# Optimization experiments

Measured on AMD Instinct MI355X. Metric: run time of the kernel, lower is better.

Reference implementation:

```python
import jax, jax.numpy as jnp
import numpy as np

N = 50000
E = 1600000
IN_F = 512
OUT_F = 128
NEG_SLOPE = 0.01   # nn.LeakyReLU() default
TEMPERATURE = 0.5


def setup_inputs() -> dict:
    key = jax.random.key(0)
    k1, k2, k3, k4 = jax.random.split(key, 4)
    h = jax.random.normal(k1, (N, IN_F), dtype=jnp.float32)
    # xavier_uniform with gain=1.414
    limW = 1.414 * np.sqrt(6.0 / (IN_F + OUT_F))
    W = jax.random.uniform(k2, (IN_F, OUT_F), minval=-limW, maxval=limW, dtype=jnp.float32)
    lima = 1.414 * np.sqrt(6.0 / (2 * OUT_F + 1))
    a = jax.random.uniform(k3, (2 * OUT_F, 1), minval=-lima, maxval=lima, dtype=jnp.float32)
    edge_index = jax.random.randint(k4, (2, E), 0, N, dtype=jnp.int64)
    return {"h": h, "W": W, "a": a, "edge_index": edge_index}


def reference(h, W, a, edge_index):
    # Inference: F.dropout(training=False) is identity.
    Wh = h @ W                                   # [N, F_out]
    src = edge_index[0]                          # row indices -> softmax segments
    dst = edge_index[1]
    # cat([Wh[src], Wh[dst]]) @ a == (Wh @ a1)[src] + (Wh @ a2)[dst]
    a1 = a[:OUT_F, 0]
    a2 = a[OUT_F:, 0]
    s1 = Wh @ a1                                 # [N]
    s2 = Wh @ a2                                 # [N]
    e = s1[src] + s2[dst]                        # [E]
    e = jnp.where(e >= 0, e, NEG_SLOPE * e)      # LeakyReLU
    logits = e / TEMPERATURE
    # sparse softmax over dim=1 (per source-node row segments)
    seg_max = jax.ops.segment_max(logits, src, num_segments=N)  # [N]
    ex = jnp.exp(logits - seg_max[src])          # [E]
    denom = jax.ops.segment_sum(ex, src, num_segments=N)        # [N]
    att = ex / denom[src]                        # [E]
    # sparse-dense matmul: h_prime[i] = sum_j att(i,j) * Wh[j]
    h_prime = jax.ops.segment_sum(att[:, None] * Wh[dst], src, num_segments=N)  # [N, F_out]
    return jax.nn.relu(h_prime)                  # concat=True path
```

## Files before the change

kernel.cpp:

```cpp
#include <hip/hip_runtime.h>
#include <cstdint>
#include <cstddef>

#define N_NODES 50000
#define N_EDGES 1600000
#define IN_FEAT 512
#define OUT_FEAT 128
#define NEG_SLOPE 0.01f
#define INV_TEMP 2.0f
#define PAD_DEG 128

#define BUCKETS 400
#define BNODES 125
#define BCAP 5000
#define A_BLOCKS 250
#define A_EPC (N_EDGES / A_BLOCKS)
#define A_G4 (A_EPC / 4)

#define CONV_BLOCKS ((IN_FEAT * OUT_FEAT) / 256)
#define GEMM_BLOCKS ((N_NODES + 63) / 64)

typedef __attribute__((ext_vector_type(8))) short short8;
typedef __attribute__((ext_vector_type(4))) float f32x4;

#define GLOBAL_AS __attribute__((address_space(1)))
#define LDS_AS __attribute__((address_space(3)))

__device__ inline unsigned short f2bf(float x) {
    unsigned int u = __float_as_uint(x);
    unsigned int r = (u + 0x7fffu + ((u >> 16) & 1u)) >> 16;
    return (unsigned short)r;
}
__device__ inline float bf2f(unsigned short b) {
    return __uint_as_float(((unsigned int)b) << 16);
}


__global__ __launch_bounds__(256) void build_kernel(const float* __restrict__ W,
                                                    unsigned short* __restrict__ Wt,
                                                    const int* __restrict__ src,
                                                    const int* __restrict__ dst,
                                                    int* __restrict__ bucket_cursor,
                                                    int* __restrict__ binned) {
    __shared__ int cntL[BUCKETS];
    __shared__ int baseL[BUCKETS];

    if (blockIdx.x >= A_BLOCKS) {
        int tid = (blockIdx.x - A_BLOCKS) * 256 + threadIdx.x;
        if (tid < IN_FEAT * OUT_FEAT) {
            int n = tid >> 9;
            int k = tid & 511;
            Wt[tid] = f2bf(W[k * OUT_FEAT + n]);
        }
        return;
    }

    int t = threadIdx.x;
    for (int i = t; i < BUCKETS; i += 256) cntL[i] = 0;
    __syncthreads();
    size_t ebase = (size_t)blockIdx.x * A_EPC;

    for (int g = t; g < A_G4; g += 256) {
        int4 s4 = *(const int4*)(src + ebase + (size_t)g * 4);
#pragma unroll
        for (int j = 0; j < 4; ++j) {
            int s = (&s4.x)[j];
            atomicAdd(&cntL[s / BNODES], 1);
        }
    }
    __syncthreads();
    for (int i = t; i < BUCKETS; i += 256) {
        int c = cntL[i];
        baseL[i] = c ? atomicAdd(&bucket_cursor[i], c) : 0;
        cntL[i] = 0;
    }
    __syncthreads();
    for (int g = t; g < A_G4; g += 256) {
        int4 s4 = *(const int4*)(src + ebase + (size_t)g * 4);
        int4 d4 = *(const int4*)(dst + ebase + (size_t)g * 4);
#pragma unroll
        for (int j = 0; j < 4; ++j) {
            int s = (&s4.x)[j];
            int b = s / BNODES;
            int sl = s - b * BNODES;
            int pos = atomicAdd(&cntL[b], 1);
            int slot = baseL[b] + pos;
            if (slot < BCAP)
                binned[(size_t)b * BCAP + slot] = (sl << 16) | (&d4.x)[j];
        }
    }
}


__global__ __launch_bounds__(256) void gemm_binB_kernel(const float* __restrict__ h,
                                                        const unsigned short* __restrict__ Wt,
                                                        const float* __restrict__ a_vec,
                                                        unsigned short* __restrict__ Whb,
                                                        float* __restrict__ s1,
                                                        float* __restrict__ s2,
                                                        const int* __restrict__ bucket_cursor,
                                                        const int* __restrict__ binned,
                                                        int* __restrict__ cnt,
                                                        int* __restrict__ csr) {
    __shared__ unsigned short lB[2][8 * 2 * 64 * 8];

    if (blockIdx.x < BUCKETS) {
        int* cL = (int*)&lB[0][0];
        int b = blockIdx.x;
        int t = threadIdx.x;
        if (t < BNODES) cL[t] = 0;
        __syncthreads();
        int m = min(bucket_cursor[b], BCAP);
        const int* bp = binned + (size_t)b * BCAP;
        int n0 = b * BNODES;
        for (int i = t; i < m; i += 256) {
            int p = bp[i];
            int sl = p >> 16;
            int d = p & 0xFFFF;
            int pos = atomicAdd(&cL[sl], 1);
            if (pos < PAD_DEG) csr[(size_t)(n0 + sl) * PAD_DEG + pos] = d;
        }
        __syncthreads();
        if (t < BNODES) cnt[n0 + t] = min(cL[t], PAD_DEG);
        return;
    }

    int bid = blockIdx.x - BUCKETS;
    int t = threadIdx.x;
    int w = t >> 6;
    int L = t & 63;
    int m0 = bid * 64;

    int arow = m0 + w * 16 + (L & 15);
    bool arow_ok = arow < N_NODES;
    int kq = (L >> 4) * 8;
    const float* arp = h + (size_t)arow * IN_FEAT + kq;

    f32x4 acc[8];
#pragma unroll
    for (int i = 0; i < 8; ++i) acc[i] = (f32x4){0.f, 0.f, 0.f, 0.f};

    auto stageB = [&](int buf, int k0) {
#pragma unroll
        for (int c = 0; c < 4; ++c) {
            int nb = w * 2 + (c >> 1);
            int ksub = c & 1;
            const GLOBAL_AS unsigned short* g =
                (const GLOBAL_AS unsigned short*)(Wt + (size_t)(nb * 16 + (L & 15)) * IN_FEAT +
                                                  (k0 + ksub * 32 + kq));
            LDS_AS unsigned short* lp = (LDS_AS unsigned short*)(&lB[buf][(nb * 2 + ksub) * 512]);
            __builtin_amdgcn_global_load_lds((const GLOBAL_AS void*)g, (LDS_AS void*)lp, 16, 0, 0);
        }
    };

    float4 av[2][2];
#pragma unroll
    for (int c = 0; c < 2; ++c) {
        av[c][0] = make_float4(0.f, 0.f, 0.f, 0.f);
        av[c][1] = make_float4(0.f, 0.f, 0.f, 0.f);
    }
    if (arow_ok) {
        av[0][0] = *(const float4*)(arp);
        av[0][1] = *(const float4*)(arp + 4);
        av[1][0] = *(const float4*)(arp + 32);
        av[1][1] = *(const float4*)(arp + 36);
    }
    stageB(0, 0);
    __syncthreads();

#pragma unroll
    for (int it = 0; it < 8; ++it) {
        const int buf = it & 1;

        if (it < 7) stageB(buf ^ 1, (it + 1) * 64);

        float4 avn[2][2];
#pragma unroll
        for (int c = 0; c < 2; ++c) {
            avn[c][0] = make_float4(0.f, 0.f, 0.f, 0.f);
            avn[c][1] = make_float4(0.f, 0.f, 0.f, 0.f);
        }
        if (it < 7 && arow_ok) {
            const float* p = arp + (it + 1) * 64;
            avn[0][0] = *(const float4*)(p);
            avn[0][1] = *(const float4*)(p + 4);
            avn[1][0] = *(const float4*)(p + 32);
            avn[1][1] = *(const float4*)(p + 36);
        }

        short8 af[2];
#pragma unroll
        for (int c = 0; c < 2; ++c) {
            short8 v;
            v[0] = (short)f2bf(av[c][0].x); v[1] = (short)f2bf(av[c][0].y);
            v[2] = (short)f2bf(av[c][0].z); v[3] = (short)f2bf(av[c][0].w);
            v[4] = (short)f2bf(av[c][1].x); v[5] = (short)f2bf(av[c][1].y);
            v[6] = (short)f2bf(av[c][1].z); v[7] = (short)f2bf(av[c][1].w);
            af[c] = v;
        }

#pragma unroll
        for (int ksub = 0; ksub < 2; ++ksub) {
#pragma unroll
            for (int nb = 0; nb < 8; ++nb) {
                short8 bf = *(const short8*)(&lB[buf][((nb * 2 + ksub) * 64 + L) * 8]);
                acc[nb] = __builtin_amdgcn_mfma_f32_16x16x32_bf16(af[ksub], bf, acc[nb], 0, 0, 0);
            }
        }

        __syncthreads();
#pragma unroll
        for (int c = 0; c < 2; ++c) {
            av[c][0] = avn[c][0];
            av[c][1] = avn[c][1];
        }
    }

    int col0 = L & 15;
    int rbase = m0 + w * 16 + (L >> 4) * 4;

    float a1c[8], a2c[8];
#pragma unroll
    for (int nb = 0; nb < 8; ++nb) {
        a1c[nb] = a_vec[nb * 16 + col0];
        a2c[nb] = a_vec[128 + nb * 16 + col0];
    }

#pragma unroll
    for (int r = 0; r < 4; ++r) {
        int row = rbase + r;
        bool ok = row < N_NODES;
        float p1 = 0.f, p2 = 0.f;
        if (ok) {
            unsigned short* orow = Whb + (size_t)row * OUT_FEAT;
#pragma unroll
            for (int nb = 0; nb < 8; ++nb) {
                float v = acc[nb][r];
                orow[nb * 16 + col0] = f2bf(v);
                p1 = fmaf(v, a1c[nb], p1);
                p2 = fmaf(v, a2c[nb], p2);
            }
        }
#pragma unroll
        for (int off = 8; off > 0; off >>= 1) {
            p1 += __shfl_xor(p1, off, 64);
            p2 += __shfl_xor(p2, off, 64);
        }
        if (ok && col0 == 0) {
            s1[row] = p1;
            s2[row] = p2;
        }
    }
}


__global__ __launch_bounds__(256) void node_kernel(const unsigned short* __restrict__ Whb,
                                                   const float* __restrict__ s1,
                                                   const float* __restrict__ s2,
                                                   const int* __restrict__ cnt,
                                                   const int* __restrict__ csr,
                                                   float* __restrict__ out) {
    int lane = threadIdx.x & 63;
    int w = threadIdx.x >> 6;
    int n = blockIdx.x * 4 + w;
    if (n >= N_NODES) return;
    int deg = cnt[n];
    size_t start = (size_t)n * PAD_DEG;
    int g = lane >> 4;
    int fo = lane & 15;

    float accv[8];
#pragma unroll
    for (int f = 0; f < 8; ++f) accv[f] = 0.f;
    float inv = 0.f;

    if (deg > 0) {
        float s1n = s1[n];
        int d0 = 0, d1 = 0;
        float ex0 = 0.f, ex1 = 0.f;
        if (lane < deg) {
            d0 = csr[start + lane];
            float ev = s1n + s2[d0];
            ev = ev >= 0.f ? ev : NEG_SLOPE * ev;
            ex0 = __expf(ev * INV_TEMP);
        }
        if (lane + 64 < deg) {
            d1 = csr[start + lane + 64];
            float ev = s1n + s2[d1];
            ev = ev >= 0.f ? ev : NEG_SLOPE * ev;
            ex1 = __expf(ev * INV_TEMP);
        }
        float denom = ex0 + ex1;
#pragma unroll
        for (int off = 32; off > 0; off >>= 1) denom += __shfl_xor(denom, off, 64);
        inv = 1.0f / denom;

#pragma unroll 2
        for (int jj = 0; jj < deg; jj += 4) {
            int e = jj + g;
            bool hi = jj >= 64;
            float exs = hi ? ex1 : ex0;
            int dsel = hi ? d1 : d0;
            float p = __shfl(exs, e & 63, 64);
            int dd = __shfl(dsel, e & 63, 64);
            short8 row = *(const short8*)(Whb + (size_t)dd * OUT_FEAT + fo * 8);
#pragma unroll
            for (int f = 0; f < 8; ++f)
                accv[f] = fmaf(p, bf2f((unsigned short)row[f]), accv[f]);
        }
#pragma unroll
        for (int f = 0; f < 8; ++f) {
            accv[f] += __shfl_xor(accv[f], 16, 64);
            accv[f] += __shfl_xor(accv[f], 32, 64);
        }
    }

    if (g == 0) {
        float* orow = out + (size_t)n * OUT_FEAT + fo * 8;
        float4 o0, o1;
        o0.x = fmaxf(accv[0] * inv, 0.f); o0.y = fmaxf(accv[1] * inv, 0.f);
        o0.z = fmaxf(accv[2] * inv, 0.f); o0.w = fmaxf(accv[3] * inv, 0.f);
        o1.x = fmaxf(accv[4] * inv, 0.f); o1.y = fmaxf(accv[5] * inv, 0.f);
        o1.z = fmaxf(accv[6] * inv, 0.f); o1.w = fmaxf(accv[7] * inv, 0.f);
        *(float4*)(orow) = o0;
        *(float4*)(orow + 4) = o1;
    }
}


extern "C" void kernel_launch(void* const* d_in, const int* in_sizes, int n_in,
                              void* d_out, int out_size, void* d_ws, size_t ws_size,
                              hipStream_t stream) {
    const float* h = (const float*)d_in[0];
    const float* W = (const float*)d_in[1];
    const float* a = (const float*)d_in[2];
    const int* edge = (const int*)d_in[3];
    const int* src = edge;
    const int* dst = edge + N_EDGES;
    float* out = (float*)d_out;

    char* ws = (char*)d_ws;
    size_t off = 0;
    auto alloc = [&](size_t bytes) -> void* {
        void* p = ws + off;
        off = (off + bytes + 255) & ~(size_t)255;
        return p;
    };
    unsigned short* Whb = (unsigned short*)alloc((size_t)N_NODES * OUT_FEAT * sizeof(unsigned short));
    float* s1 = (float*)alloc((size_t)N_NODES * sizeof(float));
    float* s2 = (float*)alloc((size_t)N_NODES * sizeof(float));
    int* cnt = (int*)alloc((size_t)N_NODES * sizeof(int));
    int* csr = (int*)alloc((size_t)N_NODES * PAD_DEG * sizeof(int));
    unsigned short* Wt = (unsigned short*)alloc((size_t)IN_FEAT * OUT_FEAT * sizeof(unsigned short));
    int* bucket_cursor = (int*)alloc((size_t)BUCKETS * sizeof(int));
    int* binned = (int*)alloc((size_t)BUCKETS * BCAP * sizeof(int));

    hipMemsetAsync(bucket_cursor, 0, BUCKETS * sizeof(int), stream);
    build_kernel<<<A_BLOCKS + CONV_BLOCKS, 256, 0, stream>>>(W, Wt, src, dst, bucket_cursor, binned);
    gemm_binB_kernel<<<BUCKETS + GEMM_BLOCKS, 256, 0, stream>>>(h, Wt, a, Whb, s1, s2,
                                                                bucket_cursor, binned, cnt, csr);
    node_kernel<<<(N_NODES + 3) / 4, 256, 0, stream>>>(Whb, s1, s2, cnt, csr, out);
}
```

Before: 262.8 us.

## Split GEMM and CSR binning kernels, load W fragments directly, unroll gather by two

```diff
diff --git a/kernel.cpp b/kernel.cpp
--- a/kernel.cpp
+++ b/kernel.cpp
@@ -92,66 +92,29 @@
 }
 
 
-__global__ __launch_bounds__(256) void gemm_binB_kernel(const float* __restrict__ h,
-                                                        const unsigned short* __restrict__ Wt,
-                                                        const float* __restrict__ a_vec,
-                                                        unsigned short* __restrict__ Whb,
-                                                        float* __restrict__ s1,
-                                                        float* __restrict__ s2,
-                                                        const int* __restrict__ bucket_cursor,
-                                                        const int* __restrict__ binned,
-                                                        int* __restrict__ cnt,
-                                                        int* __restrict__ csr) {
-    __shared__ unsigned short lB[2][8 * 2 * 64 * 8];
-
-    if (blockIdx.x < BUCKETS) {
-        int* cL = (int*)&lB[0][0];
-        int b = blockIdx.x;
-        int t = threadIdx.x;
-        if (t < BNODES) cL[t] = 0;
-        __syncthreads();
-        int m = min(bucket_cursor[b], BCAP);
-        const int* bp = binned + (size_t)b * BCAP;
-        int n0 = b * BNODES;
-        for (int i = t; i < m; i += 256) {
-            int p = bp[i];
-            int sl = p >> 16;
-            int d = p & 0xFFFF;
-            int pos = atomicAdd(&cL[sl], 1);
-            if (pos < PAD_DEG) csr[(size_t)(n0 + sl) * PAD_DEG + pos] = d;
-        }
-        __syncthreads();
-        if (t < BNODES) cnt[n0 + t] = min(cL[t], PAD_DEG);
-        return;
-    }
-
-    int bid = blockIdx.x - BUCKETS;
+__global__ __launch_bounds__(256) void gemm_kernel(const float* __restrict__ h,
+                                                   const unsigned short* __restrict__ Wt,
+                                                   const float* __restrict__ a_vec,
+                                                   unsigned short* __restrict__ Whb,
+                                                   float* __restrict__ s1,
+                                                   float* __restrict__ s2) {
+    int bid = blockIdx.x;
     int t = threadIdx.x;
     int w = t >> 6;
     int L = t & 63;
     int m0 = bid * 64;
-
-    int arow = m0 + w * 16 + (L & 15);
+    int col0 = L & 15;
+    int kq = (L >> 4) * 8;
+
+    int arow = m0 + w * 16 + col0;
     bool arow_ok = arow < N_NODES;
-    int kq = (L >> 4) * 8;
     const float* arp = h + (size_t)arow * IN_FEAT + kq;
 
+    const unsigned short* bbase = Wt + (size_t)col0 * IN_FEAT + kq;
+
     f32x4 acc[8];
 #pragma unroll
-    for (int i = 0; i < 8; ++i) acc[i] = (f32x4){0.f, 0.f, 0.f, 0.f};
-
-    auto stageB = [&](int buf, int k0) {
-#pragma unroll
-        for (int c = 0; c < 4; ++c) {
-            int nb = w * 2 + (c >> 1);
-            int ksub = c & 1;
-            const GLOBAL_AS unsigned short* g =
-                (const GLOBAL_AS unsigned short*)(Wt + (size_t)(nb * 16 + (L & 15)) * IN_FEAT +
-                                                  (k0 + ksub * 32 + kq));
-            LDS_AS unsigned short* lp = (LDS_AS unsigned short*)(&lB[buf][(nb * 2 + ksub) * 512]);
-            __builtin_amdgcn_global_load_lds((const GLOBAL_AS void*)g, (LDS_AS void*)lp, 16, 0, 0);
-        }
-    };
+    for (int nb = 0; nb < 8; ++nb) acc[nb] = (f32x4){0.f, 0.f, 0.f, 0.f};
 
     float4 av[2][2];
 #pragma unroll
@@ -165,14 +128,10 @@
         av[1][0] = *(const float4*)(arp + 32);
         av[1][1] = *(const float4*)(arp + 36);
     }
-    stageB(0, 0);
-    __syncthreads();
 
 #pragma unroll
     for (int it = 0; it < 8; ++it) {
-        const int buf = it & 1;
-
-        if (it < 7) stageB(buf ^ 1, (it + 1) * 64);
+        const int k0 = it * 64;
 
         float4 avn[2][2];
 #pragma unroll
@@ -187,6 +146,14 @@
             avn[1][0] = *(const float4*)(p + 32);
             avn[1][1] = *(const float4*)(p + 36);
         }
+
+        short8 bfr[2][8];
+#pragma unroll
+        for (int ksub = 0; ksub < 2; ++ksub)
+#pragma unroll
+            for (int nb = 0; nb < 8; ++nb)
+                bfr[ksub][nb] =
+                    *(const short8*)(bbase + (size_t)nb * 16 * IN_FEAT + k0 + ksub * 32);
 
         short8 af[2];
 #pragma unroll
@@ -200,15 +167,12 @@
         }
 
 #pragma unroll
-        for (int ksub = 0; ksub < 2; ++ksub) {
-#pragma unroll
-            for (int nb = 0; nb < 8; ++nb) {
-                short8 bf = *(const short8*)(&lB[buf][((nb * 2 + ksub) * 64 + L) * 8]);
-                acc[nb] = __builtin_amdgcn_mfma_f32_16x16x32_bf16(af[ksub], bf, acc[nb], 0, 0, 0);
-            }
-        }
-
-        __syncthreads();
+        for (int ksub = 0; ksub < 2; ++ksub)
+#pragma unroll
+            for (int nb = 0; nb < 8; ++nb)
+                acc[nb] = __builtin_amdgcn_mfma_f32_16x16x32_bf16(af[ksub], bfr[ksub][nb],
+                                                                  acc[nb], 0, 0, 0);
+
 #pragma unroll
         for (int c = 0; c < 2; ++c) {
             av[c][0] = avn[c][0];
@@ -216,9 +180,6 @@
         }
     }
 
-    int col0 = L & 15;
-    int rbase = m0 + w * 16 + (L >> 4) * 4;
-
     float a1c[8], a2c[8];
 #pragma unroll
     for (int nb = 0; nb < 8; ++nb) {
@@ -226,6 +187,7 @@
         a2c[nb] = a_vec[128 + nb * 16 + col0];
     }
 
+    int rbase = m0 + w * 16 + (L >> 4) * 4;
 #pragma unroll
     for (int r = 0; r < 4; ++r) {
         int row = rbase + r;
@@ -251,6 +213,30 @@
             s2[row] = p2;
         }
     }
+}
+
+
+__global__ __launch_bounds__(256) void binB_kernel(const int* __restrict__ bucket_cursor,
+                                                   const int* __restrict__ binned,
+                                                   int* __restrict__ cnt,
+                                                   int* __restrict__ csr) {
+    __shared__ int cL[BNODES];
+    int b = blockIdx.x;
+    int t = threadIdx.x;
+    if (t < BNODES) cL[t] = 0;
+    __syncthreads();
+    int m = min(bucket_cursor[b], BCAP);
+    const int* bp = binned + (size_t)b * BCAP;
+    int n0 = b * BNODES;
+    for (int i = t; i < m; i += 256) {
+        int p = bp[i];
+        int sl = p >> 16;
+        int d = p & 0xFFFF;
+        int pos = atomicAdd(&cL[sl], 1);
+        if (pos < PAD_DEG) csr[(size_t)(n0 + sl) * PAD_DEG + pos] = d;
+    }
+    __syncthreads();
+    if (t < BNODES) cnt[n0 + t] = min(cL[t], PAD_DEG);
 }
 
 
@@ -296,17 +282,23 @@
         inv = 1.0f / denom;
 
 #pragma unroll 2
-        for (int jj = 0; jj < deg; jj += 4) {
-            int e = jj + g;
-            bool hi = jj >= 64;
-            float exs = hi ? ex1 : ex0;
-            int dsel = hi ? d1 : d0;
-            float p = __shfl(exs, e & 63, 64);
-            int dd = __shfl(dsel, e & 63, 64);
-            short8 row = *(const short8*)(Whb + (size_t)dd * OUT_FEAT + fo * 8);
+        for (int jj = 0; jj < deg; jj += 8) {
+            int e0 = jj + g;
+            int e1 = jj + 4 + g;
+            bool hi0 = jj >= 64;
+            bool hi1 = (jj + 4) >= 64;
+            float p0 = __shfl(hi0 ? ex1 : ex0, e0 & 63, 64);
+            int dd0 = __shfl(hi0 ? d1 : d0, e0 & 63, 64);
+            float p1 = __shfl(hi1 ? ex1 : ex0, e1 & 63, 64);
+            int dd1 = __shfl(hi1 ? d1 : d0, e1 & 63, 64);
+            short8 row0 = *(const short8*)(Whb + (size_t)dd0 * OUT_FEAT + fo * 8);
+            short8 row1 = *(const short8*)(Whb + (size_t)dd1 * OUT_FEAT + fo * 8);
 #pragma unroll
             for (int f = 0; f < 8; ++f)
-                accv[f] = fmaf(p, bf2f((unsigned short)row[f]), accv[f]);
+                accv[f] = fmaf(p0, bf2f((unsigned short)row0[f]), accv[f]);
+#pragma unroll
+            for (int f = 0; f < 8; ++f)
+                accv[f] = fmaf(p1, bf2f((unsigned short)row1[f]), accv[f]);
         }
 #pragma unroll
         for (int f = 0; f < 8; ++f) {
@@ -357,7 +349,7 @@
 
     hipMemsetAsync(bucket_cursor, 0, BUCKETS * sizeof(int), stream);
     build_kernel<<<A_BLOCKS + CONV_BLOCKS, 256, 0, stream>>>(W, Wt, src, dst, bucket_cursor, binned);
-    gemm_binB_kernel<<<BUCKETS + GEMM_BLOCKS, 256, 0, stream>>>(h, Wt, a, Whb, s1, s2,
-                                                                bucket_cursor, binned, cnt, csr);
+    gemm_kernel<<<GEMM_BLOCKS, 256, 0, stream>>>(h, Wt, a, Whb, s1, s2);
+    binB_kernel<<<BUCKETS, 256, 0, stream>>>(bucket_cursor, binned, cnt, csr);
     node_kernel<<<(N_NODES + 3) / 4, 256, 0, stream>>>(Whb, s1, s2, cnt, csr, out);
 }
```

Measured after the change: 297.3 us. 13.1% more time.
